# Optimization experiments

Hardware: AMD Instinct MI355X
Metric: run time of the kernel (lower is better)

Reference implementation:

```python
import jax, jax.numpy as jnp
import numpy as np

EPS = 1e-12
N_HEADS = 16


def _ln(x, g, b, eps=EPS):
    m = jnp.mean(x, axis=-1, keepdims=True)
    v = jnp.var(x, axis=-1, keepdims=True)
    return (x - m) * jax.lax.rsqrt(v + eps) * g + b


def setup_inputs() -> dict:
    key = jax.random.key(0)
    ks = jax.random.split(key, 8)
    B, S, D, I = 2, 2048, 1024, 4096
    s = 0.02
    f32 = jnp.float32
    return {
        "x": jax.random.normal(ks[0], (B, S, D), f32),
        "input_mask": jnp.zeros((B, 1, 1, S), f32),  # additive mask, 0 = no masking
        "norm_w": jnp.ones((D,), f32),
        "norm_b": jnp.zeros((D,), f32),
        "attn_qkvw": jax.random.normal(ks[1], (D, 3 * D), f32) * s,
        "attn_qkvb": jnp.zeros((3 * D,), f32),
        "attn_ow": jax.random.normal(ks[2], (D, D), f32) * s,
        "attn_ob": jnp.zeros((D,), f32),
        "attn_nw": jnp.ones((D,), f32),
        "attn_nb": jnp.zeros((D,), f32),
        "inter_w": jax.random.normal(ks[3], (D, I), f32) * s,
        "inter_b": jnp.zeros((I,), f32),
        "inter_w1": jax.random.normal(ks[4], (D, I), f32) * s,
        "output_w": jax.random.normal(ks[5], (I, D), f32) * s,
        "output_b": jnp.zeros((D,), f32),
    }


def reference(x, input_mask, norm_w, norm_b, attn_qkvw, attn_qkvb, attn_ow,
              attn_ob, attn_nw, attn_nb, inter_w, inter_b, inter_w1,
              output_w, output_b):
    B, S, D = x.shape
    hd = D // N_HEADS

    # --- fused qkv_gemm: pre-layernorm + QKV GEMM + bias ---
    ln1 = _ln(x, norm_w, norm_b)
    qkv = ln1 @ attn_qkvw + attn_qkvb            # [B,S,3D]
    q, k, v = jnp.split(qkv, 3, axis=-1)

    def to_heads(t):  # [B,S,D] -> [B,H,S,hd]
        return t.reshape(B, S, N_HEADS, hd).transpose(0, 2, 1, 3)

    q, k, v = to_heads(q), to_heads(k), to_heads(v)

    # --- softmax-context attention (scale_attention=True -> 1/sqrt(head_dim)) ---
    scores = jnp.einsum('bhqd,bhkd->bhqk', q, k) / jnp.sqrt(jnp.float32(hd))
    scores = scores + input_mask                 # additive mask [B,1,1,S]
    probs = jax.nn.softmax(scores, axis=-1)
    ctx = jnp.einsum('bhqk,bhkd->bhqd', probs, v)
    ctx = ctx.transpose(0, 2, 1, 3).reshape(B, S, D)

    attn_out = ctx @ attn_ow                     # vector_matmul (no bias)

    # --- fused mlp_gemm: bias+residual add, layernorm, GEMM+bias+gelu ---
    residual_add = attn_out + attn_ob + x
    ln2 = _ln(residual_add, attn_nw, attn_nb)
    intermediate = jax.nn.gelu(ln2 @ inter_w + inter_b, approximate=False)
    # gated path: vector_matmul(mlp input, inter_w1) * intermediate (per source)
    intermediate = (attn_out @ inter_w1) * intermediate

    # --- output projection + bias_residual ---
    out = intermediate @ output_w + output_b + residual_add
    return out
```

## Files before the change

### kernel.cpp

```cpp
#include <hip/hip_runtime.h>
#include <hip/hip_bf16.h>

#define BATCH 2
#define SEQ   2048
#define DIM   1024
#define IDIM  4096
#define NH    16
#define HD    64
#define TOK   (BATCH * SEQ)

typedef __hip_bfloat16 bf16;

typedef short bf16x8_t __attribute__((ext_vector_type(8)));
typedef float f32x4_t  __attribute__((ext_vector_type(4)));

__device__ __forceinline__ float ldv(const float* p, size_t i) { return p[i]; }
__device__ __forceinline__ float ldv(const bf16*  p, size_t i) { return __bfloat162float(p[i]); }
__device__ __forceinline__ void  stv(float* p, size_t i, float v) { p[i] = v; }
__device__ __forceinline__ void  stv(bf16*  p, size_t i, float v) { p[i] = __float2bfloat16(v); }

__device__ __forceinline__ f32x4_t mfma16(bf16x8_t a, bf16x8_t b, f32x4_t c) {
    return __builtin_amdgcn_mfma_f32_16x16x32_bf16(a, b, c, 0, 0, 0);
}

__device__ __forceinline__ void gload16(const bf16* g, bf16* l) {
    __builtin_amdgcn_global_load_lds(
        (const __attribute__((address_space(1))) void*)g,
        (__attribute__((address_space(3))) void*)l, 16, 0, 0);
}

__device__ __forceinline__ void xcd_map(int &bx, int &by) {
    const int gn  = gridDim.x;
    const int lin = blockIdx.y * gn + blockIdx.x;
    const int cx  = gn >> 3;
    const int xcd = lin & 7;
    const int slot = lin >> 3;
    bx = xcd * cx + slot % cx;
    by = slot / cx;
}

__global__ __launch_bounds__(256) void ln_kernel(const float* __restrict__ in,
                                                 const float* __restrict__ w,
                                                 const float* __restrict__ b,
                                                 bf16* __restrict__ out) {
    const int row = blockIdx.x;
    const int tid = threadIdx.x;
    const float* xr = in + (size_t)row * DIM;

    float v[4], sum = 0.f, sq = 0.f;
#pragma unroll
    for (int i = 0; i < 4; i++) {
        float t = xr[tid + i * 256];
        v[i] = t; sum += t; sq += t * t;
    }
#pragma unroll
    for (int off = 32; off >= 1; off >>= 1) {
        sum += __shfl_xor(sum, off);
        sq  += __shfl_xor(sq,  off);
    }
    __shared__ float s1[4], s2[4];
    int wid = tid >> 6;
    if ((tid & 63) == 0) { s1[wid] = sum; s2[wid] = sq; }
    __syncthreads();
    sum = s1[0] + s1[1] + s1[2] + s1[3];
    sq  = s2[0] + s2[1] + s2[2] + s2[3];

    const float mean = sum * (1.f / DIM);
    const float var  = fmaxf(sq * (1.f / DIM) - mean * mean, 0.f);
    const float rstd = rsqrtf(var + 1e-12f);

    bf16* orow = out + (size_t)row * DIM;
#pragma unroll
    for (int i = 0; i < 4; i++) {
        int idx = tid + i * 256;
        orow[idx] = __float2bfloat16((v[i] - mean) * rstd * w[idx] + b[idx]);
    }
}

__global__ __launch_bounds__(256) void wconv_kernel(const float* __restrict__ W,
                                                    bf16* __restrict__ Wt,
                                                    int K, int N) {
    __shared__ float tile[32][33];
    const int tid = threadIdx.x;
    const int n0 = blockIdx.x * 32;
    const int k0 = blockIdx.y * 32;
    const int c = tid & 31;
    const int r = tid >> 5;
#pragma unroll
    for (int i = 0; i < 4; i++)
        tile[r + i * 8][c] = W[(size_t)(k0 + r + i * 8) * N + n0 + c];
    __syncthreads();
#pragma unroll
    for (int i = 0; i < 4; i++)
        Wt[(size_t)(n0 + r + i * 8) * K + k0 + c] = __float2bfloat16(tile[c][r + i * 8]);
}

#define GBK 32

template<typename TX, int MODE, int TM, int TN>
__global__ __launch_bounds__(256) void mgemm_kernel(const bf16* __restrict__ A,
                                                    const bf16* __restrict__ Bt,
                                                    const float* __restrict__ bias,
                                                    const TX* __restrict__ aux,
                                                    TX* __restrict__ C,
                                                    const float* __restrict__ bias2,
                                                    const float* __restrict__ xin,
                                                    float* __restrict__ C2,
                                                    int M, int N, int K) {
    constexpr int TILE_M = TM * 32;
    constexpr int TILE_N = TN * 32;
    constexpr int LOADS  = TM / 2 + TN / 2;
    __shared__ alignas(16) bf16 As[2][TILE_M][GBK];
    __shared__ alignas(16) bf16 Bs[2][TILE_N][GBK];

    const int tid  = threadIdx.x;
    const int w    = tid >> 6;
    const int lane = tid & 63;
    const int cl   = lane & 15;
    const int qd   = lane >> 4;
    const int wm   = w >> 1;
    const int wn   = w & 1;

    int bx, by;
    xcd_map(bx, by);

    const int row0 = by * TILE_M;
    const int col0 = bx * TILE_N;

    const int lrow = lane >> 2;
    const int lkg  = lane & 3;
    const int sslot = lkg ^ ((lrow >> 1) & 3);
    const int rds   = (cl >> 1) & 3;

    const bf16* gA = A  + (size_t)(row0 + lrow) * K + sslot * 8;
    const bf16* gB = Bt + (size_t)(col0 + lrow) * K + sslot * 8;

    f32x4_t acc[TM][TN];
#pragma unroll
    for (int m = 0; m < TM; m++)
#pragma unroll
        for (int n = 0; n < TN; n++) acc[m][n] = {0.f, 0.f, 0.f, 0.f};

    auto stage = [&](int b, int k0) {
#pragma unroll
        for (int i = 0; i < TM / 2; i++) {
            const int r16 = (w * (TM / 2) + i) * 16;
            gload16(gA + (size_t)r16 * K + k0, &As[b][r16][0]);
        }
#pragma unroll
        for (int j = 0; j < TN / 2; j++) {
            const int r16 = (w * (TN / 2) + j) * 16;
            gload16(gB + (size_t)r16 * K + k0, &Bs[b][r16][0]);
        }
    };

    stage(0, 0);
    stage(1, GBK);
    asm volatile("s_waitcnt vmcnt(%0)" :: "i"(LOADS) : "memory");
    __builtin_amdgcn_s_barrier();

    const int NT = K / GBK;
    for (int t = 0; t < NT; t++) {
        const int cur = t & 1;

        bf16x8_t af[TM], bfr[TN];
#pragma unroll
        for (int m = 0; m < TM; m++)
            af[m] = *(const bf16x8_t*)&As[cur][wm * (TM * 16) + m * 16 + cl][(qd ^ rds) * 8];
#pragma unroll
        for (int n = 0; n < TN; n++)
            bfr[n] = *(const bf16x8_t*)&Bs[cur][wn * (TN * 16) + n * 16 + cl][(qd ^ rds) * 8];
        asm volatile("s_waitcnt lgkmcnt(0)" ::: "memory");
        __builtin_amdgcn_sched_barrier(0);
        __builtin_amdgcn_s_barrier();

        if (t + 2 < NT) stage(cur, (t + 2) * GBK);

        __builtin_amdgcn_s_setprio(1);
#pragma unroll
        for (int m = 0; m < TM; m++)
#pragma unroll
            for (int n = 0; n < TN; n++)
                acc[m][n] = mfma16(af[m], bfr[n], acc[m][n]);
        __builtin_amdgcn_s_setprio(0);

        if (t + 1 < NT) {
            if (t + 2 < NT)
                asm volatile("s_waitcnt vmcnt(%0)" :: "i"(LOADS) : "memory");
            else
                asm volatile("s_waitcnt vmcnt(0)" ::: "memory");
            __builtin_amdgcn_s_barrier();
        }
    }

#pragma unroll
    for (int m = 0; m < TM; m++) {
#pragma unroll
        for (int n = 0; n < TN; n++) {
            const int gc = col0 + wn * (TN * 16) + n * 16 + cl;
            const float bv = (MODE != 4 && bias) ? bias[gc] : 0.f;
#pragma unroll
            for (int r = 0; r < 4; r++) {
                const int gr = row0 + wm * (TM * 16) + m * 16 + qd * 4 + r;
                float c = acc[m][n][r] + bv;
                if (MODE == 3) {
                    c += ldv(aux, (size_t)gr * N + gc);
                }
                stv(C, (size_t)gr * N + gc, c);
                if (MODE == 4) {
                    C2[(size_t)gr * N + gc] = c + bias2[gc] + xin[(size_t)gr * N + gc];
                }
            }
        }
    }
}

template<int TM, int TN>
__global__ __launch_bounds__(256) void dualgemm_kernel(const bf16* __restrict__ A0,
                                                       const bf16* __restrict__ B0t,
                                                       const bf16* __restrict__ A1,
                                                       const bf16* __restrict__ B1t,
                                                       const float* __restrict__ bias,
                                                       bf16* __restrict__ C,
                                                       int M, int N, int K) {
    constexpr int TILE_M = TM * 32;
    constexpr int TILE_N = TN * 32;
    constexpr int LOADS  = TM + TN;
    __shared__ alignas(16) bf16 As0[2][TILE_M][GBK];
    __shared__ alignas(16) bf16 Bs0[2][TILE_N][GBK];
    __shared__ alignas(16) bf16 As1[2][TILE_M][GBK];
    __shared__ alignas(16) bf16 Bs1[2][TILE_N][GBK];

    const int tid  = threadIdx.x;
    const int w    = tid >> 6;
    const int lane = tid & 63;
    const int cl   = lane & 15;
    const int qd   = lane >> 4;
    const int wm   = w >> 1;
    const int wn   = w & 1;

    int bx, by;
    xcd_map(bx, by);

    const int row0 = by * TILE_M;
    const int col0 = bx * TILE_N;

    const int lrow = lane >> 2;
    const int lkg  = lane & 3;
    const int sslot = lkg ^ ((lrow >> 1) & 3);
    const int rds   = (cl >> 1) & 3;

    const bf16* gA0 = A0  + (size_t)(row0 + lrow) * K + sslot * 8;
    const bf16* gB0 = B0t + (size_t)(col0 + lrow) * K + sslot * 8;
    const bf16* gA1 = A1  + (size_t)(row0 + lrow) * K + sslot * 8;
    const bf16* gB1 = B1t + (size_t)(col0 + lrow) * K + sslot * 8;

    f32x4_t acc0[TM][TN], acc1[TM][TN];
#pragma unroll
    for (int m = 0; m < TM; m++)
#pragma unroll
        for (int n = 0; n < TN; n++) {
            acc0[m][n] = {0.f, 0.f, 0.f, 0.f};
            acc1[m][n] = {0.f, 0.f, 0.f, 0.f};
        }

    auto stage = [&](int b, int k0) {
#pragma unroll
        for (int i = 0; i < TM / 2; i++) {
            const int r16 = (w * (TM / 2) + i) * 16;
            gload16(gA0 + (size_t)r16 * K + k0, &As0[b][r16][0]);
            gload16(gA1 + (size_t)r16 * K + k0, &As1[b][r16][0]);
        }
#pragma unroll
        for (int j = 0; j < TN / 2; j++) {
            const int r16 = (w * (TN / 2) + j) * 16;
            gload16(gB0 + (size_t)r16 * K + k0, &Bs0[b][r16][0]);
            gload16(gB1 + (size_t)r16 * K + k0, &Bs1[b][r16][0]);
        }
    };

    stage(0, 0);
    stage(1, GBK);
    asm volatile("s_waitcnt vmcnt(%0)" :: "i"(LOADS) : "memory");
    __builtin_amdgcn_s_barrier();

    const int NT = K / GBK;
    for (int t = 0; t < NT; t++) {
        const int cur = t & 1;

        bf16x8_t af0[TM], af1[TM], bf0[TN], bf1[TN];
#pragma unroll
        for (int m = 0; m < TM; m++) {
            const int rr = wm * (TM * 16) + m * 16 + cl;
            af0[m] = *(const bf16x8_t*)&As0[cur][rr][(qd ^ rds) * 8];
            af1[m] = *(const bf16x8_t*)&As1[cur][rr][(qd ^ rds) * 8];
        }
#pragma unroll
        for (int n = 0; n < TN; n++) {
            const int rr = wn * (TN * 16) + n * 16 + cl;
            bf0[n] = *(const bf16x8_t*)&Bs0[cur][rr][(qd ^ rds) * 8];
            bf1[n] = *(const bf16x8_t*)&Bs1[cur][rr][(qd ^ rds) * 8];
        }
        asm volatile("s_waitcnt lgkmcnt(0)" ::: "memory");
        __builtin_amdgcn_sched_barrier(0);
        __builtin_amdgcn_s_barrier();

        if (t + 2 < NT) stage(cur, (t + 2) * GBK);

        __builtin_amdgcn_s_setprio(1);
#pragma unroll
        for (int n = 0; n < TN; n++)
#pragma unroll
            for (int m = 0; m < TM; m++) {
                acc0[m][n] = mfma16(af0[m], bf0[n], acc0[m][n]);
                acc1[m][n] = mfma16(af1[m], bf1[n], acc1[m][n]);
            }
        __builtin_amdgcn_s_setprio(0);

        if (t + 1 < NT) {
            if (t + 2 < NT)
                asm volatile("s_waitcnt vmcnt(%0)" :: "i"(LOADS) : "memory");
            else
                asm volatile("s_waitcnt vmcnt(0)" ::: "memory");
            __builtin_amdgcn_s_barrier();
        }
    }

#pragma unroll
    for (int m = 0; m < TM; m++) {
#pragma unroll
        for (int n = 0; n < TN; n++) {
            const int gc = col0 + wn * (TN * 16) + n * 16 + cl;
            const float bv = bias[gc];
#pragma unroll
            for (int r = 0; r < 4; r++) {
                const int gr = row0 + wm * (TM * 16) + m * 16 + qd * 4 + r;
                float g = acc0[m][n][r] + bv;
                g = 0.5f * g * (1.f + erff(g * 0.70710678118654752f));
                C[(size_t)gr * N + gc] = __float2bfloat16(g * acc1[m][n][r]);
            }
        }
    }
}

__global__ __launch_bounds__(256) void vtrans_kernel(const bf16* __restrict__ qkv,
                                                     bf16* __restrict__ vt) {
    __shared__ bf16 t[64][72];
    const int tid = threadIdx.x;
    const int s0  = blockIdx.x * 64;
    const int bh  = blockIdx.y;
    const int bb  = bh >> 4;
    const int h   = bh & 15;
    const bf16* src = qkv + (size_t)bb * SEQ * (3 * DIM) + 2 * DIM + h * HD;
    const int r  = tid >> 3;
    const int cc = tid & 7;
#pragma unroll
    for (int i = 0; i < 2; i++)
        *(bf16x8_t*)&t[r + i * 32][cc * 8] =
            *(const bf16x8_t*)(src + (size_t)(s0 + r + i * 32) * (3 * DIM) + cc * 8);
    __syncthreads();
    bf16* dst = vt + (size_t)bh * HD * SEQ + s0;
#pragma unroll
    for (int i = 0; i < 2; i++) {
        const int d = r + i * 32;
        bf16x8_t v;
#pragma unroll
        for (int j = 0; j < 8; j++)
            ((short*)&v)[j] = *(const short*)&t[cc * 8 + j][d];
        *(bf16x8_t*)(dst + (size_t)d * SEQ + cc * 8) = v;
    }
}

#define KCH 64
#define NCH (SEQ / KCH)

__device__ __forceinline__ unsigned pk2(float lo, float hi) {
    unsigned a = (unsigned)__bfloat16_as_ushort(__float2bfloat16(lo));
    unsigned b = (unsigned)__bfloat16_as_ushort(__float2bfloat16(hi));
    return a | (b << 16);
}

union PAU { bf16x8_t v; unsigned u[4]; };

__global__ __launch_bounds__(256, 2) void attn_mfma_kernel(const bf16* __restrict__ qkv,
                                                           const bf16* __restrict__ vt,
                                                           const float* __restrict__ mask,
                                                           bf16* __restrict__ ctx) {
    __shared__ alignas(16) bf16 Kl[2][KCH][64];
    __shared__ alignas(16) bf16 Vl[2][KCH][64];

    const int tid  = threadIdx.x;
    const int w    = tid >> 6;
    const int lane = tid & 63;
    const int cl   = lane & 15;
    const int qd   = lane >> 4;
    const int c7   = cl & 7;

    const int qtile = blockIdx.x;
    const int bh    = blockIdx.y;
    const int bb    = bh >> 4;
    const int h     = bh & 15;

    const bf16*  base = qkv + (size_t)bb * SEQ * (3 * DIM) + h * HD;
    const bf16*  gK   = base + DIM;
    const bf16*  gV   = vt + (size_t)bh * HD * SEQ;
    const float* mrow = mask + (size_t)bb * SEQ;

    bf16x8_t aq[2][2];
#pragma unroll
    for (int qt = 0; qt < 2; qt++) {
        const bf16* qrow = base + (size_t)(qtile * 128 + w * 32 + qt * 16 + cl) * (3 * DIM);
        aq[qt][0] = *(const bf16x8_t*)(qrow + qd * 8);
        aq[qt][1] = *(const bf16x8_t*)(qrow + 32 + qd * 8);
    }

    const bf16x8_t onesv = {0x3F80, 0x3F80, 0x3F80, 0x3F80,
                            0x3F80, 0x3F80, 0x3F80, 0x3F80};

    const int sr  = lane >> 3;
    const int scw = (lane & 7) ^ sr;

#pragma unroll
    for (int i = 0; i < 2; i++) {
        const int row = i * 32 + w * 8 + sr;
        gload16(gK + (size_t)row * (3 * DIM) + scw * 8, &Kl[0][i * 32 + w * 8][0]);
        gload16(gV + (size_t)row * SEQ + scw * 8, &Vl[0][i * 32 + w * 8][0]);
    }
    f32x4_t mkx[4];
#pragma unroll
    for (int ks = 0; ks < 4; ks++)
        mkx[ks] = *(const f32x4_t*)&mrow[ks * 16 + qd * 4];

    f32x4_t O[2][4];
#pragma unroll
    for (int qt = 0; qt < 2; qt++)
#pragma unroll
        for (int ns = 0; ns < 4; ns++) O[qt][ns] = {0.f, 0.f, 0.f, 0.f};
    f32x4_t li[2] = {{0.f,0.f,0.f,0.f},{0.f,0.f,0.f,0.f}};

    for (int c = 0; c < NCH; c++) {
        __syncthreads();
        const bf16 (*Kb)[64] = Kl[c & 1];
        const bf16 (*Vb)[64] = Vl[c & 1];

        f32x4_t mk[4];
#pragma unroll
        for (int ks = 0; ks < 4; ks++) mk[ks] = mkx[ks];

        if (c + 1 < NCH) {
            bf16 (*Kn)[64] = Kl[(c + 1) & 1];
            bf16 (*Vn)[64] = Vl[(c + 1) & 1];
            const int k0n = (c + 1) * KCH;
#pragma unroll
            for (int i = 0; i < 2; i++) {
                const int row = i * 32 + w * 8 + sr;
                gload16(gK + (size_t)(k0n + row) * (3 * DIM) + scw * 8, &Kn[i * 32 + w * 8][0]);
                gload16(gV + (size_t)row * SEQ + k0n + scw * 8, &Vn[i * 32 + w * 8][0]);
            }
#pragma unroll
            for (int ks = 0; ks < 4; ks++)
                mkx[ks] = *(const f32x4_t*)&mrow[k0n + ks * 16 + qd * 4];
        }

        bf16x8_t kf[4][2];
#pragma unroll
        for (int ks = 0; ks < 4; ks++) {
            kf[ks][0] = *(const bf16x8_t*)&Kb[ks * 16 + cl][(qd ^ c7) << 3];
            kf[ks][1] = *(const bf16x8_t*)&Kb[ks * 16 + cl][((4 + qd) ^ c7) << 3];
        }

        PAU pa[2][2];
#pragma unroll
        for (int qt = 0; qt < 2; qt++) {
            unsigned Dv[4][2];
#pragma unroll
            for (int ks = 0; ks < 4; ks++) {
                f32x4_t s = {0.f, 0.f, 0.f, 0.f};
                s = mfma16(kf[ks][0], aq[qt][0], s);
                s = mfma16(kf[ks][1], aq[qt][1], s);
                const float e0 = __expf(s[0] * 0.125f + mk[ks][0]);
                const float e1 = __expf(s[1] * 0.125f + mk[ks][1]);
                const float e2 = __expf(s[2] * 0.125f + mk[ks][2]);
                const float e3 = __expf(s[3] * 0.125f + mk[ks][3]);
                Dv[ks][0] = pk2(e0, e1);
                Dv[ks][1] = pk2(e2, e3);
            }
#pragma unroll
            for (int rp = 0; rp < 2; rp++) {
                auto z0 = __builtin_amdgcn_permlane32_swap(Dv[0][rp], Dv[1][rp], false, false);
                auto w0 = __builtin_amdgcn_permlane16_swap(z0[0], z0[1], false, false);
                pa[qt][0].u[rp]     = w0[0];
                pa[qt][0].u[rp + 2] = w0[1];
                auto z1 = __builtin_amdgcn_permlane32_swap(Dv[2][rp], Dv[3][rp], false, false);
                auto w1 = __builtin_amdgcn_permlane16_swap(z1[0], z1[1], false, false);
                pa[qt][1].u[rp]     = w1[0];
                pa[qt][1].u[rp + 2] = w1[1];
            }
            f32x4_t ls = {0.f, 0.f, 0.f, 0.f};
            ls = mfma16(pa[qt][0].v, onesv, ls);
            ls = mfma16(pa[qt][1].v, onesv, ls);
            li[qt] += ls;
        }

#pragma unroll
        for (int ns = 0; ns < 4; ns++) {
            bf16x8_t v0 = *(const bf16x8_t*)&Vb[ns * 16 + cl][(qd ^ c7) << 3];
            bf16x8_t v1 = *(const bf16x8_t*)&Vb[ns * 16 + cl][((4 + qd) ^ c7) << 3];
#pragma unroll
            for (int qt = 0; qt < 2; qt++) {
                O[qt][ns] = mfma16(pa[qt][0].v, v0, O[qt][ns]);
                O[qt][ns] = mfma16(pa[qt][1].v, v1, O[qt][ns]);
            }
        }
    }

#pragma unroll
    for (int qt = 0; qt < 2; qt++) {
#pragma unroll
        for (int r = 0; r < 4; r++) {
            const int row = qtile * 128 + w * 32 + qt * 16 + qd * 4 + r;
            bf16* orow = ctx + (size_t)(bb * SEQ + row) * DIM + h * HD;
            const float inv = 1.f / li[qt][r];
#pragma unroll
            for (int ns = 0; ns < 4; ns++)
                orow[ns * 16 + cl] = __float2bfloat16(O[qt][ns][r] * inv);
        }
    }
}

extern "C" void kernel_launch(void* const* d_in, const int* in_sizes, int n_in,
                              void* d_out, int out_size, void* d_ws, size_t ws_size,
                              hipStream_t stream) {
    const float* x        = (const float*)d_in[0];
    const float* mask     = (const float*)d_in[1];
    const float* norm_w   = (const float*)d_in[2];
    const float* norm_b   = (const float*)d_in[3];
    const float* qkvw     = (const float*)d_in[4];
    const float* qkvb     = (const float*)d_in[5];
    const float* attn_ow  = (const float*)d_in[6];
    const float* attn_ob  = (const float*)d_in[7];
    const float* attn_nw  = (const float*)d_in[8];
    const float* attn_nb  = (const float*)d_in[9];
    const float* inter_w  = (const float*)d_in[10];
    const float* inter_b  = (const float*)d_in[11];
    const float* inter_w1 = (const float*)d_in[12];
    const float* output_w = (const float*)d_in[13];
    const float* output_b = (const float*)d_in[14];

    float* out = (float*)d_out;
    bf16*  ws  = (bf16*)d_ws;

    const size_t M1 = 1024 * 1024;
    bf16* ln_s      = ws;
    bf16* qkv       = ws + 4 * M1;
    bf16* inter     = ws + 4 * M1;
    bf16* qkvw_t    = ws + 16 * M1;
    bf16* attn_owt  = ws + 19 * M1;
    bf16* vt        = ws + 20 * M1;
    bf16* attn_out  = ws + 20 * M1;
    bf16* inter_wt  = ws + 24 * M1;
    bf16* inter_w1t = ws + 28 * M1;
    bf16* output_wt = ws + 32 * M1;
    float* resid    = out;

    dim3 blk(256);

    wconv_kernel<<<dim3(3072 / 32, 1024 / 32), blk, 0, stream>>>(qkvw,     qkvw_t,    1024, 3072);
    wconv_kernel<<<dim3(1024 / 32, 1024 / 32), blk, 0, stream>>>(attn_ow,  attn_owt,  1024, 1024);
    wconv_kernel<<<dim3(4096 / 32, 1024 / 32), blk, 0, stream>>>(inter_w,  inter_wt,  1024, 4096);
    wconv_kernel<<<dim3(4096 / 32, 1024 / 32), blk, 0, stream>>>(inter_w1, inter_w1t, 1024, 4096);
    wconv_kernel<<<dim3(1024 / 32, 4096 / 32), blk, 0, stream>>>(output_w, output_wt, 4096, 1024);

    ln_kernel<<<TOK, blk, 0, stream>>>(x, norm_w, norm_b, ln_s);

    mgemm_kernel<bf16, 0, 4, 4><<<dim3(3072 / 128, TOK / 128), blk, 0, stream>>>(
        ln_s, qkvw_t, qkvb, (const bf16*)nullptr, qkv,
        nullptr, nullptr, nullptr, TOK, 3 * DIM, DIM);

    vtrans_kernel<<<dim3(SEQ / 64, BATCH * NH), blk, 0, stream>>>(qkv, vt);

    attn_mfma_kernel<<<dim3(SEQ / 128, BATCH * NH), blk, 0, stream>>>(qkv, vt, mask, ln_s);

    mgemm_kernel<bf16, 4, 4, 2><<<dim3(DIM / 64, TOK / 128), blk, 0, stream>>>(
        ln_s, attn_owt, (const float*)nullptr, (const bf16*)nullptr, attn_out,
        attn_ob, x, resid, TOK, DIM, DIM);

    ln_kernel<<<TOK, blk, 0, stream>>>(resid, attn_nw, attn_nb, ln_s);

    dualgemm_kernel<4, 4><<<dim3(IDIM / 128, TOK / 128), blk, 0, stream>>>(
        ln_s, inter_wt, attn_out, inter_w1t, inter_b, inter, TOK, IDIM, DIM);

    mgemm_kernel<float, 3, 4, 2><<<dim3(DIM / 64, TOK / 128), blk, 0, stream>>>(
        inter, output_wt, output_b, resid, out,
        nullptr, nullptr, nullptr, TOK, DIM, IDIM);
}
```

Measured before the change: 495.9 us.

## Split dual GEMM across two 4-wave groups with LDS exchange for gated epilogue

```diff
diff --git a/kernel.cpp b/kernel.cpp
--- a/kernel.cpp
+++ b/kernel.cpp
@@ -215,92 +215,80 @@
     }
 }
 
-template<int TM, int TN>
-__global__ __launch_bounds__(256) void dualgemm_kernel(const bf16* __restrict__ A0,
-                                                       const bf16* __restrict__ B0t,
-                                                       const bf16* __restrict__ A1,
-                                                       const bf16* __restrict__ B1t,
-                                                       const float* __restrict__ bias,
-                                                       bf16* __restrict__ C,
-                                                       int M, int N, int K) {
-    constexpr int TILE_M = TM * 32;
-    constexpr int TILE_N = TN * 32;
-    constexpr int LOADS  = TM + TN;
-    __shared__ alignas(16) bf16 As0[2][TILE_M][GBK];
-    __shared__ alignas(16) bf16 Bs0[2][TILE_N][GBK];
-    __shared__ alignas(16) bf16 As1[2][TILE_M][GBK];
-    __shared__ alignas(16) bf16 Bs1[2][TILE_N][GBK];
+__global__ __launch_bounds__(512, 4) void dualgemm_kernel(const bf16* __restrict__ A0,
+                                                          const bf16* __restrict__ B0t,
+                                                          const bf16* __restrict__ A1,
+                                                          const bf16* __restrict__ B1t,
+                                                          const float* __restrict__ bias,
+                                                          bf16* __restrict__ C,
+                                                          int M, int N, int K) {
+    __shared__ alignas(16) char pool[66560];
 
     const int tid  = threadIdx.x;
     const int w    = tid >> 6;
     const int lane = tid & 63;
     const int cl   = lane & 15;
     const int qd   = lane >> 4;
-    const int wm   = w >> 1;
-    const int wn   = w & 1;
+    const int gsel = w >> 2;
+    const int g2   = w & 3;
+    const int wm   = g2 >> 1;
+    const int wn   = g2 & 1;
 
     int bx, by;
     xcd_map(bx, by);
-
-    const int row0 = by * TILE_M;
-    const int col0 = bx * TILE_N;
+    const int row0 = by * 128;
+    const int col0 = bx * 128;
 
     const int lrow = lane >> 2;
     const int lkg  = lane & 3;
     const int sslot = lkg ^ ((lrow >> 1) & 3);
     const int rds   = (cl >> 1) & 3;
 
-    const bf16* gA0 = A0  + (size_t)(row0 + lrow) * K + sslot * 8;
-    const bf16* gB0 = B0t + (size_t)(col0 + lrow) * K + sslot * 8;
-    const bf16* gA1 = A1  + (size_t)(row0 + lrow) * K + sslot * 8;
-    const bf16* gB1 = B1t + (size_t)(col0 + lrow) * K + sslot * 8;
-
-    f32x4_t acc0[TM][TN], acc1[TM][TN];
-#pragma unroll
-    for (int m = 0; m < TM; m++)
-#pragma unroll
-        for (int n = 0; n < TN; n++) {
-            acc0[m][n] = {0.f, 0.f, 0.f, 0.f};
-            acc1[m][n] = {0.f, 0.f, 0.f, 0.f};
-        }
+    const int sarr = w >> 1;
+    const bf16* gsrc;
+    {
+        const bf16* bases[4] = {A0, B0t, A1, B1t};
+        const int   r0s[4]   = {row0, col0, row0, col0};
+        gsrc = bases[sarr] + (size_t)(r0s[sarr] + lrow) * K + sslot * 8;
+    }
+
+    auto sptr = [&](int b, int a) -> bf16* {
+        return (bf16*)(pool + b * 32768 + a * 8192);
+    };
+
+    f32x4_t acc[4][4];
+#pragma unroll
+    for (int m = 0; m < 4; m++)
+#pragma unroll
+        for (int n = 0; n < 4; n++) acc[m][n] = {0.f, 0.f, 0.f, 0.f};
 
     auto stage = [&](int b, int k0) {
-#pragma unroll
-        for (int i = 0; i < TM / 2; i++) {
-            const int r16 = (w * (TM / 2) + i) * 16;
-            gload16(gA0 + (size_t)r16 * K + k0, &As0[b][r16][0]);
-            gload16(gA1 + (size_t)r16 * K + k0, &As1[b][r16][0]);
-        }
-#pragma unroll
-        for (int j = 0; j < TN / 2; j++) {
-            const int r16 = (w * (TN / 2) + j) * 16;
-            gload16(gB0 + (size_t)r16 * K + k0, &Bs0[b][r16][0]);
-            gload16(gB1 + (size_t)r16 * K + k0, &Bs1[b][r16][0]);
+        bf16* dst = sptr(b, sarr);
+#pragma unroll
+        for (int j = 0; j < 4; j++) {
+            const int rg = (w & 1) * 4 + j;
+            gload16(gsrc + (size_t)(rg * 16) * K + k0, dst + rg * 16 * GBK);
         }
     };
 
     stage(0, 0);
     stage(1, GBK);
-    asm volatile("s_waitcnt vmcnt(%0)" :: "i"(LOADS) : "memory");
+    asm volatile("s_waitcnt vmcnt(4)" ::: "memory");
     __builtin_amdgcn_s_barrier();
 
     const int NT = K / GBK;
     for (int t = 0; t < NT; t++) {
         const int cur = t & 1;
-
-        bf16x8_t af0[TM], af1[TM], bf0[TN], bf1[TN];
-#pragma unroll
-        for (int m = 0; m < TM; m++) {
-            const int rr = wm * (TM * 16) + m * 16 + cl;
-            af0[m] = *(const bf16x8_t*)&As0[cur][rr][(qd ^ rds) * 8];
-            af1[m] = *(const bf16x8_t*)&As1[cur][rr][(qd ^ rds) * 8];
-        }
-#pragma unroll
-        for (int n = 0; n < TN; n++) {
-            const int rr = wn * (TN * 16) + n * 16 + cl;
-            bf0[n] = *(const bf16x8_t*)&Bs0[cur][rr][(qd ^ rds) * 8];
-            bf1[n] = *(const bf16x8_t*)&Bs1[cur][rr][(qd ^ rds) * 8];
-        }
+        const bf16* Sa = sptr(cur, gsel * 2);
+        const bf16* Sb = sptr(cur, gsel * 2 + 1);
+
+        bf16x8_t af[4], bfr[4];
+#pragma unroll
+        for (int m = 0; m < 4; m++)
+            af[m] = *(const bf16x8_t*)&Sa[(wm * 64 + m * 16 + cl) * GBK + (qd ^ rds) * 8];
+#pragma unroll
+        for (int n = 0; n < 4; n++)
+            bfr[n] = *(const bf16x8_t*)&Sb[(wn * 64 + n * 16 + cl) * GBK + (qd ^ rds) * 8];
         asm volatile("s_waitcnt lgkmcnt(0)" ::: "memory");
         __builtin_amdgcn_sched_barrier(0);
         __builtin_amdgcn_s_barrier();
@@ -309,35 +297,49 @@
 
         __builtin_amdgcn_s_setprio(1);
 #pragma unroll
-        for (int n = 0; n < TN; n++)
-#pragma unroll
-            for (int m = 0; m < TM; m++) {
-                acc0[m][n] = mfma16(af0[m], bf0[n], acc0[m][n]);
-                acc1[m][n] = mfma16(af1[m], bf1[n], acc1[m][n]);
-            }
+        for (int m = 0; m < 4; m++)
+#pragma unroll
+            for (int n = 0; n < 4; n++)
+                acc[m][n] = mfma16(af[m], bfr[n], acc[m][n]);
         __builtin_amdgcn_s_setprio(0);
 
         if (t + 1 < NT) {
             if (t + 2 < NT)
-                asm volatile("s_waitcnt vmcnt(%0)" :: "i"(LOADS) : "memory");
+                asm volatile("s_waitcnt vmcnt(4)" ::: "memory");
             else
                 asm volatile("s_waitcnt vmcnt(0)" ::: "memory");
             __builtin_amdgcn_s_barrier();
         }
     }
 
-#pragma unroll
-    for (int m = 0; m < TM; m++) {
-#pragma unroll
-        for (int n = 0; n < TN; n++) {
-            const int gc = col0 + wn * (TN * 16) + n * 16 + cl;
-            const float bv = bias[gc];
-#pragma unroll
-            for (int r = 0; r < 4; r++) {
-                const int gr = row0 + wm * (TM * 16) + m * 16 + qd * 4 + r;
-                float g = acc0[m][n][r] + bv;
-                g = 0.5f * g * (1.f + erff(g * 0.70710678118654752f));
-                C[(size_t)gr * N + gc] = __float2bfloat16(g * acc1[m][n][r]);
+    float* X = (float*)pool;
+    __syncthreads();
+    if (gsel == 1) {
+#pragma unroll
+        for (int m = 0; m < 4; m++)
+#pragma unroll
+            for (int n = 0; n < 4; n++)
+#pragma unroll
+                for (int r = 0; r < 4; r++)
+                    X[(wm * 64 + m * 16 + qd * 4 + r) * 130 + wn * 64 + n * 16 + cl] =
+                        acc[m][n][r];
+    }
+    __syncthreads();
+    if (gsel == 0) {
+#pragma unroll
+        for (int m = 0; m < 4; m++) {
+#pragma unroll
+            for (int n = 0; n < 4; n++) {
+                const int lc = wn * 64 + n * 16 + cl;
+                const int gc = col0 + lc;
+                const float bv = bias[gc];
+#pragma unroll
+                for (int r = 0; r < 4; r++) {
+                    const int lr = wm * 64 + m * 16 + qd * 4 + r;
+                    float g = acc[m][n][r] + bv;
+                    g = 0.5f * g * (1.f + erff(g * 0.70710678118654752f));
+                    C[(size_t)(row0 + lr) * N + gc] = __float2bfloat16(g * X[lr * 130 + lc]);
+                }
             }
         }
     }
@@ -587,7 +589,7 @@
 
     ln_kernel<<<TOK, blk, 0, stream>>>(resid, attn_nw, attn_nb, ln_s);
 
-    dualgemm_kernel<4, 4><<<dim3(IDIM / 128, TOK / 128), blk, 0, stream>>>(
+    dualgemm_kernel<<<dim3(IDIM / 128, TOK / 128), dim3(512), 0, stream>>>(
         ln_s, inter_wt, attn_out, inter_w1t, inter_b, inter, TOK, IDIM, DIM);
 
     mgemm_kernel<float, 3, 4, 2><<<dim3(DIM / 64, TOK / 128), blk, 0, stream>>>(
```

New measurement: 449.9 us. 9.3% less time.
